# Kernel tuning notes

Hardware: AMD Instinct MI355X
Metric: run time of the kernel (lower is better)

Reference implementation:

```python
import jax, jax.numpy as jnp
import numpy as np

B, N, E, H = 8, 1500, 3000, 256
HOPS = 3


def setup_inputs() -> dict:
    key = jax.random.key(0)
    ks = jax.random.split(key, 9)
    node_state = jax.random.normal(ks[0], (B, N, H), jnp.float32)
    edge_vec = jax.random.normal(ks[1], (B, E, H), jnp.float32)
    # sparse-ish 0/1 incidence matrices (avg ~3 nonzeros per row)
    node2edge = (jax.random.uniform(ks[2], (B, E, N)) < 0.002).astype(jnp.float32)
    edge2node = (jax.random.uniform(ks[3], (B, N, E)) < 0.002).astype(jnp.float32)
    s = 1.0 / np.sqrt(H).astype(np.float32)
    W_max = jax.random.uniform(ks[4], (H, H), jnp.float32, -s, s)        # linear_max, no bias
    W_fz = jax.random.uniform(ks[5], (4 * H, H), jnp.float32, -s, s)     # gated fusion
    b_fz = jnp.zeros((H,), jnp.float32)
    W_z = jax.random.uniform(ks[6], (2 * H, H), jnp.float32, -s, s)      # GRU gates, no bias
    W_r = jax.random.uniform(ks[7], (2 * H, H), jnp.float32, -s, s)
    W_t = jax.random.uniform(ks[8], (2 * H, H), jnp.float32, -s, s)
    return dict(node_state=node_state, edge_vec=edge_vec, node2edge=node2edge,
                edge2node=edge2node, W_max=W_max, W_fz=W_fz, b_fz=b_fz,
                W_z=W_z, W_r=W_r, W_t=W_t)


def _msg_pass(node_state, edge_vec, n2e, e2n):
    # n2e: (B,E,N), e2n: (B,N,E)
    edge_emb = jnp.einsum('ben,bnh->beh', n2e, node_state) + edge_vec   # (B,E,H)
    norm = jnp.sum(e2n, axis=2, keepdims=True) + 1.0                     # self-loop degree norm
    return (jnp.einsum('bne,beh->bnh', e2n, edge_emb) + node_state) / norm


def _gated_fusion(h, x, W_fz, b_fz):
    z = jax.nn.sigmoid(jnp.concatenate([h, x, h * x, h - x], -1) @ W_fz + b_fz)
    return (1.0 - z) * h + z * x


def _gru_step(h, x, W_z, W_r, W_t):
    hx = jnp.concatenate([h, x], -1)
    z = jax.nn.sigmoid(hx @ W_z)
    r = jax.nn.sigmoid(hx @ W_r)
    t = jnp.tanh(jnp.concatenate([r * h, x], -1) @ W_t)
    return (1.0 - z) * h + z * t


def reference(node_state, edge_vec, node2edge, edge2node, W_max, W_fz, b_fz, W_z, W_r, W_t):
    n2e_T = jnp.swapaxes(node2edge, 1, 2)   # (B,N,E)
    e2n_T = jnp.swapaxes(edge2node, 1, 2)   # (B,E,N)
    for _ in range(HOPS):
        bw = _msg_pass(node_state, edge_vec, node2edge, edge2node)
        fw = _msg_pass(node_state, edge_vec, e2n_T, n2e_T)
        agg = _gated_fusion(fw, bw, W_fz, b_fz)
        node_state = _gru_step(node_state, agg, W_z, W_r, W_t)
    # graph max pool: linear then max over nodes
    graph_embedding = jnp.max(node_state @ W_max, axis=1)[None]  # (1,B,H)
    return jnp.swapaxes(node_state, 0, 1), graph_embedding       # (N,B,H), (1,B,H)
```

## Files before the change

### kernel.cpp

```cpp
#include <hip/hip_runtime.h>
#include <hip/hip_bf16.h>
#include <stdint.h>

#define Bb 8
#define Nn 1500
#define Ee 3000
#define Hh 256
#define NHOPS 3
#define CAP 32
#define Mrows (Bb*Nn)
#define BE (Bb*Ee)
#define BN (Bb*Nn)
#define TOTQ 9000000

typedef __bf16 bf16x8 __attribute__((ext_vector_type(8)));
typedef float f32x4 __attribute__((ext_vector_type(4)));

__device__ __forceinline__ float sigmoidf_(float x){ return 1.f/(1.f+__expf(-x)); }

__device__ __forceinline__ unsigned short f2b(float f){
  union { float f; unsigned int u; } x; x.f = f;
  unsigned int r = (x.u + 0x7fffu + ((x.u >> 16) & 1u)) >> 16;
  return (unsigned short)r;
}
__device__ __forceinline__ float b2f(unsigned short u){
  union { unsigned int u; float f; } x; x.u = ((unsigned int)u) << 16;
  return x.f;
}
__device__ __forceinline__ ushort4 pack4(float4 v){
  return make_ushort4(f2b(v.x), f2b(v.y), f2b(v.z), f2b(v.w));
}
__device__ __forceinline__ float4 unpack4(ushort4 u){
  return make_float4(b2f(u.x), b2f(u.y), b2f(u.z), b2f(u.w));
}
__device__ __forceinline__ unsigned fkey(float f){
  unsigned u = __float_as_uint(f);
  return (u & 0x80000000u) ? ~u : (u | 0x80000000u);
}

#define GLL16(g, l) __builtin_amdgcn_global_load_lds( \
    (const __attribute__((address_space(1))) unsigned int*)(g), \
    (__attribute__((address_space(3))) unsigned int*)(l), 16, 0, 0)

__device__ __forceinline__ void scan_proc(float4 vv, int t,
    int* __restrict__ Aidx, int* __restrict__ cntA, int* __restrict__ Didx, int* __restrict__ cntD,
    int* __restrict__ Bidx, int* __restrict__ cntB, int* __restrict__ Cidx, int* __restrict__ cntC) {
  if (vv.x == 0.f && vv.y == 0.f && vv.z == 0.f && vv.w == 0.f) return;
  int *rowIdx, *rowCnt, *colIdx, *colCnt;
  int g, q, R, C;
  if (t < TOTQ) {
    rowIdx = Aidx; rowCnt = cntA; colIdx = Didx; colCnt = cntD;
    R = Ee; C = Nn;
    g = t / 375; q = t - g * 375;
  } else {
    int tt = t - TOTQ;
    rowIdx = Bidx; rowCnt = cntB; colIdx = Cidx; colCnt = cntC;
    R = Nn; C = Ee;
    g = tt / 750; q = tt - g * 750;
  }
  int b = g / R;
  int r = g - b * R;
  int cbase = q * 4;
  #pragma unroll
  for (int j = 0; j < 4; ++j) {
    float vj = (j == 0) ? vv.x : (j == 1) ? vv.y : (j == 2) ? vv.z : vv.w;
    if (vj != 0.f) {
      int c = cbase + j;
      int rs = atomicAdd(&rowCnt[g], 1);
      if (rs < CAP) rowIdx[(size_t)g * CAP + rs] = c;
      int cs = atomicAdd(&colCnt[b * C + c], 1);
      if (cs < CAP) colIdx[(size_t)(b * C + c) * CAP + cs] = r;
    }
  }
}

__global__ void scan_kernel(const float4* __restrict__ n2e4, const float4* __restrict__ e2n4,
                            int* __restrict__ Aidx, int* __restrict__ cntA,
                            int* __restrict__ Didx, int* __restrict__ cntD,
                            int* __restrict__ Bidx, int* __restrict__ cntB,
                            int* __restrict__ Cidx, int* __restrict__ cntC) {
  int t0 = blockIdx.x * 1024 + threadIdx.x;
  float4 v[4];
  int ts[4];
  #pragma unroll
  for (int r2 = 0; r2 < 4; ++r2) {
    int t = t0 + r2 * 256;
    ts[r2] = t;
    const float4* p = (t < TOTQ) ? (n2e4 + t) : (e2n4 + (t - TOTQ));
    v[r2] = (t < 2 * TOTQ) ? *p : make_float4(0.f, 0.f, 0.f, 0.f);
  }
  __builtin_amdgcn_sched_barrier(0);
  #pragma unroll
  for (int r2 = 0; r2 < 4; ++r2)
    scan_proc(v[r2], ts[r2], Aidx, cntA, Didx, cntD, Bidx, cntB, Cidx, cntC);
}

__global__ void prep_kernel(const float* __restrict__ Wfz, const float* __restrict__ Wz,
                            const float* __restrict__ Wr, const float* __restrict__ Wt,
                            const float* __restrict__ Wmax,
                            unsigned short* __restrict__ WfzT, unsigned short* __restrict__ WzrT,
                            unsigned short* __restrict__ WtT, unsigned short* __restrict__ WmaxT,
                            const float* __restrict__ in_ns, unsigned short* __restrict__ nsb,
                            const float* __restrict__ in_ev, unsigned short* __restrict__ evb) {
  int bx = blockIdx.x;
  if (bx < 2560) {
    int t = bx * 256 + threadIdx.x;
    if (t < 196608) {
      int n = t / 768, k = t % 768;
      float v;
      if (k < 256)      v = Wfz[k * 256 + n] + Wfz[(k + 768) * 256 + n];
      else if (k < 512) v = Wfz[k * 256 + n] - Wfz[(k + 512) * 256 + n];
      else              v = Wfz[k * 256 + n];
      WfzT[t] = f2b(v);
    } else if (t < 458752) {
      int u = t - 196608;
      int j = u >> 9, k = u & 511;
      float v = (j < 256) ? Wz[k * 256 + j] : Wr[k * 256 + (j - 256)];
      WzrT[u] = f2b(v);
    } else if (t < 589824) {
      int u = t - 458752;
      int n = u >> 9, k = u & 511;
      WtT[u] = f2b(Wt[k * 256 + n]);
    } else if (t < 655360) {
      int u = t - 589824;
      int n = u >> 8, k = u & 255;
      WmaxT[u] = f2b(Wmax[k * 256 + n]);
    }
  } else if (bx < 3310) {
    int t0 = (bx - 2560) * 1024 + threadIdx.x;
    #pragma unroll
    for (int r = 0; r < 4; ++r) {
      int t = t0 + r * 256;
      ((ushort4*)nsb)[t] = pack4(((const float4*)in_ns)[t]);
    }
  } else {
    int t0 = (bx - 3310) * 1024 + threadIdx.x;
    #pragma unroll
    for (int r = 0; r < 4; ++r) {
      int t = t0 + r * 256;
      ((ushort4*)evb)[t] = pack4(((const float4*)in_ev)[t]);
    }
  }
}

__device__ __forceinline__ void sort_one(int* pp, int c) {
  if (c > CAP) c = CAP;
  int v[CAP];
  for (int j = 0; j < c; ++j) v[j] = pp[j];
  for (int j = 1; j < c; ++j) { int key = v[j]; int k = j - 1;
    while (k >= 0 && v[k] > key) { v[k+1] = v[k]; --k; } v[k+1] = key; }
  for (int j = 0; j < c; ++j) pp[j] = v[j];
}
__global__ void sort4_kernel(int* __restrict__ Cidx, const int* __restrict__ cntC,
                             int* __restrict__ Didx, const int* __restrict__ cntD,
                             int* __restrict__ Aidx, const int* __restrict__ cntA,
                             int* __restrict__ Bidx, const int* __restrict__ cntB) {
  int i = blockIdx.x * 256 + threadIdx.x;
  if (i < BE) sort_one(Cidx + (size_t)i * CAP, cntC[i]);
  else if (i < BE + BN) { int k = i - BE; sort_one(Didx + (size_t)k * CAP, cntD[k]); }
  else if (i < 2 * BE + BN) { int k = i - BE - BN; sort_one(Aidx + (size_t)k * CAP, cntA[k]); }
  else if (i < 2 * BE + 2 * BN) { int k = i - 2 * BE - BN; sort_one(Bidx + (size_t)k * CAP, cntB[k]); }
}

__global__ void edge_kernel(const ushort4* __restrict__ evb4, const ushort4* __restrict__ nsb4,
                            const int* __restrict__ Aidx, const int* __restrict__ Acnt,
                            const int* __restrict__ Cidx, const int* __restrict__ Ccnt,
                            ushort4* __restrict__ eb4, ushort4* __restrict__ ef4) {
  int w = __builtin_amdgcn_readfirstlane((int)(threadIdx.x >> 6));
  int be = blockIdx.x * 4 + w;
  int lane = threadIdx.x & 63;
  int b = be / Ee;
  int cA = min(Acnt[be], CAP), cC = min(Ccnt[be], CAP);
  const int* pA = Aidx + (size_t)be * CAP;
  const int* pC = Cidx + (size_t)be * CAP;
  float4 ev = unpack4(evb4[(size_t)be * 64 + lane]);
  float4 sA = ev, sC = ev;
  for (int i = 0; i < cA; ++i) {
    int n = pA[i];
    float4 t = unpack4(nsb4[((size_t)b * Nn + n) * 64 + lane]);
    sA.x += t.x; sA.y += t.y; sA.z += t.z; sA.w += t.w;
  }
  for (int i = 0; i < cC; ++i) {
    int n = pC[i];
    float4 t = unpack4(nsb4[((size_t)b * Nn + n) * 64 + lane]);
    sC.x += t.x; sC.y += t.y; sC.z += t.z; sC.w += t.w;
  }
  eb4[(size_t)be * 64 + lane] = pack4(sA);
  ef4[(size_t)be * 64 + lane] = pack4(sC);
}

__global__ void node_kernel(const float4* __restrict__ nsin4,
                            const ushort4* __restrict__ eb4, const ushort4* __restrict__ ef4,
                            const int* __restrict__ Bidx, const int* __restrict__ Bcnt,
                            const int* __restrict__ Didx, const int* __restrict__ Dcnt,
                            ushort4* __restrict__ Xfz4, ushort4* __restrict__ Xzr4) {
  int w = __builtin_amdgcn_readfirstlane((int)(threadIdx.x >> 6));
  int bn = blockIdx.x * 4 + w;
  int lane = threadIdx.x & 63;
  int b = bn / Nn;
  int rB = Bcnt[bn], rD = Dcnt[bn];
  int cB = min(rB, CAP), cD = min(rD, CAP);
  const int* pB = Bidx + (size_t)bn * CAP;
  const int* pD = Didx + (size_t)bn * CAP;
  float4 h0 = nsin4[(size_t)bn * 64 + lane];
  float4 sb = h0, sf = h0;
  for (int i = 0; i < cB; ++i) {
    int e = pB[i];
    float4 t = unpack4(eb4[((size_t)b * Ee + e) * 64 + lane]);
    sb.x += t.x; sb.y += t.y; sb.z += t.z; sb.w += t.w;
  }
  for (int i = 0; i < cD; ++i) {
    int e = pD[i];
    float4 t = unpack4(ef4[((size_t)b * Ee + e) * 64 + lane]);
    sf.x += t.x; sf.y += t.y; sf.z += t.z; sf.w += t.w;
  }
  float ib = 1.f / (1.f + (float)rB), idf = 1.f / (1.f + (float)rD);
  sb.x *= ib; sb.y *= ib; sb.z *= ib; sb.w *= ib;
  sf.x *= idf; sf.y *= idf; sf.z *= idf; sf.w *= idf;
  float4 prod = make_float4(sf.x*sb.x, sf.y*sb.y, sf.z*sb.z, sf.w*sb.w);
  size_t m = bn;
  Xfz4[m * 192 +   0 + lane] = pack4(sf);
  Xfz4[m * 192 +  64 + lane] = pack4(sb);
  Xfz4[m * 192 + 128 + lane] = pack4(prod);
  Xzr4[m * 128 + lane] = pack4(h0);
}

#define EPI_FZ   1
#define EPI_ZR   2
#define EPI_GRU  3
#define EPI_MAX  4

template<int EPI, int LAST>
__global__ __launch_bounds__(512) void gemm_kernel(
    const unsigned short* __restrict__ A, const unsigned short* __restrict__ WT,
    int M, int K,
    unsigned* __restrict__ gkey, const float* __restrict__ bfz,
    unsigned short* __restrict__ Xzr, unsigned short* __restrict__ zbuf,
    unsigned short* __restrict__ Xt,
    const float* __restrict__ nsin, float* __restrict__ nsout,
    unsigned short* __restrict__ nsbout)
{
  __shared__ unsigned short As[128 * 64];
  __shared__ unsigned short Bs[64 * 64];
  int m0 = blockIdx.x * 128, n0 = blockIdx.y * 64;
  int tid = threadIdx.x;
  int lane = tid & 63;
  int wid = __builtin_amdgcn_readfirstlane(tid >> 6);
  int wm = wid >> 1, wn = wid & 1;
  int p = lane >> 4;
  int q = lane & 7;
  int lr = lane >> 3;
  f32x4 acc[2][2] = {};
  for (int k0 = 0; k0 < K; k0 += 64) {
    {
      int rl0 = wid * 16 + lr;
      int gm0 = m0 + rl0; if (gm0 > M - 1) gm0 = M - 1;
      GLL16(A + (size_t)gm0 * K + k0 + ((q ^ (rl0 & 7)) << 3), &As[(wid * 16) * 64]);
      int rl1 = rl0 + 8;
      int gm1 = m0 + rl1; if (gm1 > M - 1) gm1 = M - 1;
      GLL16(A + (size_t)gm1 * K + k0 + ((q ^ (rl1 & 7)) << 3), &As[(wid * 16 + 8) * 64]);
      int rb = wid * 8 + lr;
      GLL16(WT + (size_t)(n0 + rb) * K + k0 + ((q ^ (rb & 7)) << 3), &Bs[(wid * 8) * 64]);
    }
    __syncthreads();
    #pragma unroll
    for (int kk = 0; kk < 64; kk += 32) {
      int cq = (kk >> 3) + p;
      int ra0 = wm * 32 + (lane & 15);
      int ra1 = ra0 + 16;
      int rb0 = wn * 32 + (lane & 15);
      int rb1 = rb0 + 16;
      bf16x8 a0 = *(const bf16x8*)&As[ra0 * 64 + ((cq ^ (ra0 & 7)) << 3)];
      bf16x8 a1 = *(const bf16x8*)&As[ra1 * 64 + ((cq ^ (ra1 & 7)) << 3)];
      bf16x8 b0 = *(const bf16x8*)&Bs[rb0 * 64 + ((cq ^ (rb0 & 7)) << 3)];
      bf16x8 b1 = *(const bf16x8*)&Bs[rb1 * 64 + ((cq ^ (rb1 & 7)) << 3)];
      acc[0][0] = __builtin_amdgcn_mfma_f32_16x16x32_bf16(a0, b0, acc[0][0], 0, 0, 0);
      acc[0][1] = __builtin_amdgcn_mfma_f32_16x16x32_bf16(a0, b1, acc[0][1], 0, 0, 0);
      acc[1][0] = __builtin_amdgcn_mfma_f32_16x16x32_bf16(a1, b0, acc[1][0], 0, 0, 0);
      acc[1][1] = __builtin_amdgcn_mfma_f32_16x16x32_bf16(a1, b1, acc[1][1], 0, 0, 0);
    }
    __syncthreads();
  }
  if (EPI == EPI_MAX) {
    #pragma unroll
    for (int mi = 0; mi < 2; ++mi)
    #pragma unroll
    for (int ni = 0; ni < 2; ++ni) {
      int mb = m0 + wm * 32 + mi * 16 + p * 4;
      int c = n0 + wn * 32 + ni * 16 + (lane & 15);
      if (mb >= M) continue;
      int b0 = mb / Nn, b3 = (mb + 3) / Nn;
      if (b0 == b3) {
        float mx = fmaxf(fmaxf(acc[mi][ni][0], acc[mi][ni][1]),
                         fmaxf(acc[mi][ni][2], acc[mi][ni][3]));
        atomicMax(&gkey[b0 * 256 + c], fkey(mx));
      } else {
        #pragma unroll
        for (int j = 0; j < 4; ++j)
          atomicMax(&gkey[((mb + j) / Nn) * 256 + c], fkey(acc[mi][ni][j]));
      }
    }
    return;
  }
  #pragma unroll
  for (int mi = 0; mi < 2; ++mi)
  #pragma unroll
  for (int ni = 0; ni < 2; ++ni)
  #pragma unroll
  for (int j = 0; j < 4; ++j) {
    int m = m0 + wm * 32 + mi * 16 + p * 4 + j;
    int c = n0 + wn * 32 + ni * 16 + (lane & 15);
    if (m >= M) continue;
    float v = acc[mi][ni][j];
    if (EPI == EPI_FZ) {
      float z = sigmoidf_(v + bfz[c]);
      float fw = b2f(A[(size_t)m * K + c]);
      float bw = b2f(A[(size_t)m * K + 256 + c]);
      unsigned short agg = f2b((1.f - z) * fw + z * bw);
      Xzr[(size_t)m * 512 + 256 + c] = agg;
      Xt[(size_t)m * 512 + 256 + c] = agg;
    } else if (EPI == EPI_ZR) {
      float s = sigmoidf_(v);
      if (c < 256) {
        zbuf[(size_t)m * 256 + c] = f2b(s);
      } else {
        int cz = c - 256;
        Xt[(size_t)m * 512 + cz] = f2b(s * nsin[(size_t)m * 256 + cz]);
      }
    } else {
      float t = tanhf(v);
      float zz = b2f(zbuf[(size_t)m * 256 + c]);
      float h = nsin[(size_t)m * 256 + c];
      float nh = (1.f - zz) * h + zz * t;
      nsbout[(size_t)m * 256 + c] = f2b(nh);
      if (LAST) {
        int bb = m / Nn, n = m - bb * Nn;
        nsout[((size_t)n * Bb + bb) * 256 + c] = nh;
      } else {
        nsout[(size_t)m * 256 + c] = nh;
      }
    }
  }
}

__global__ void maxfin_kernel(const unsigned* __restrict__ gkey, float* __restrict__ out) {
  int t = blockIdx.x * 256 + threadIdx.x;
  if (t >= Bb * Hh) return;
  unsigned k = gkey[t];
  unsigned u = (k & 0x80000000u) ? (k & 0x7fffffffu) : ~k;
  out[(size_t)Nn * Bb * Hh + t] = __uint_as_float(u);
}

extern "C" void kernel_launch(void* const* d_in, const int* in_sizes, int n_in,
                              void* d_out, int out_size, void* d_ws, size_t ws_size,
                              hipStream_t stream) {
  const float* in_ns   = (const float*)d_in[0];
  const float* in_ev   = (const float*)d_in[1];
  const float* in_n2e  = (const float*)d_in[2];
  const float* in_e2n  = (const float*)d_in[3];
  const float* in_wmax = (const float*)d_in[4];
  const float* in_wfz  = (const float*)d_in[5];
  const float* in_bfz  = (const float*)d_in[6];
  const float* in_wz   = (const float*)d_in[7];
  const float* in_wr   = (const float*)d_in[8];
  const float* in_wt   = (const float*)d_in[9];
  float* out = (float*)d_out;

  char* base = (char*)d_ws;
  size_t off = 0;
  auto alloc = [&](size_t bytes) -> void* {
    void* r = base + off;
    off = (off + bytes + 255) & ~(size_t)255;
    return r;
  };
  int* cnts = (int*)alloc((size_t)(2 * BE + 2 * BN) * 4);
  unsigned* gkey = (unsigned*)alloc(Bb * Hh * 4);
  int* cntC = cnts;
  int* cntD = cnts + BE;
  int* cntA = cnts + BE + BN;
  int* cntB = cnts + BE + BN + BE;
  int* Aidx = (int*)alloc((size_t)BE * CAP * 4);
  int* Bidx = (int*)alloc((size_t)BN * CAP * 4);
  int* Cidx = (int*)alloc((size_t)BE * CAP * 4);
  int* Didx = (int*)alloc((size_t)BN * CAP * 4);
  float* ns   = (float*)alloc((size_t)Mrows * Hh * 4);
  unsigned short* nsb = (unsigned short*)alloc((size_t)Mrows * Hh * 2);
  unsigned short* evb = (unsigned short*)alloc((size_t)BE * Hh * 2);
  unsigned short* eb = (unsigned short*)alloc((size_t)BE * Hh * 2);
  unsigned short* ef = (unsigned short*)alloc((size_t)BE * Hh * 2);
  unsigned short* Xfz = (unsigned short*)alloc((size_t)Mrows * 768 * 2);
  unsigned short* Xzr = (unsigned short*)alloc((size_t)Mrows * 512 * 2);
  unsigned short* Xt  = (unsigned short*)alloc((size_t)Mrows * 512 * 2);
  unsigned short* zbuf = (unsigned short*)alloc((size_t)Mrows * 256 * 2);
  unsigned short* WfzT  = (unsigned short*)alloc(256 * 768 * 2);
  unsigned short* WzrT  = (unsigned short*)alloc(512 * 512 * 2);
  unsigned short* WtT   = (unsigned short*)alloc(256 * 512 * 2);
  unsigned short* WmaxT = (unsigned short*)alloc(256 * 256 * 2);
  (void)ws_size; (void)in_sizes; (void)n_in; (void)out_size;

  hipMemsetAsync(cnts, 0, (size_t)(2 * BE + 2 * BN) * 4 + (size_t)Bb * Hh * 4, stream);

  scan_kernel<<<(2 * TOTQ + 1023) / 1024, 256, 0, stream>>>(
      (const float4*)in_n2e, (const float4*)in_e2n,
      Aidx, cntA, Didx, cntD, Bidx, cntB, Cidx, cntC);
  prep_kernel<<<4810, 256, 0, stream>>>(
      in_wfz, in_wz, in_wr, in_wt, in_wmax,
      WfzT, WzrT, WtT, WmaxT,
      in_ns, nsb, in_ev, evb);
  sort4_kernel<<<(2 * BE + 2 * BN + 255) / 256, 256, 0, stream>>>(
      Cidx, cntC, Didx, cntD, Aidx, cntA, Bidx, cntB);

  dim3 gFZ(94, 4), gZR(94, 8), gT(94, 4);
  for (int hop = 0; hop < NHOPS; ++hop) {
    const float* nsin = (hop == 0) ? in_ns : ns;
    edge_kernel<<<BE / 4, 256, 0, stream>>>((const ushort4*)evb, (const ushort4*)nsb,
        Aidx, cntA, Cidx, cntC, (ushort4*)eb, (ushort4*)ef);
    node_kernel<<<BN / 4, 256, 0, stream>>>((const float4*)nsin,
        (const ushort4*)eb, (const ushort4*)ef,
        Bidx, cntB, Didx, cntD, (ushort4*)Xfz, (ushort4*)Xzr);
    gemm_kernel<EPI_FZ, 0><<<gFZ, 512, 0, stream>>>(Xfz, WfzT, Mrows, 768,
        nullptr, in_bfz, Xzr, nullptr, Xt, nullptr, nullptr, nullptr);
    gemm_kernel<EPI_ZR, 0><<<gZR, 512, 0, stream>>>(Xzr, WzrT, Mrows, 512,
        nullptr, nullptr, nullptr, zbuf, Xt, nsin, nullptr, nullptr);
    if (hop < NHOPS - 1) {
      gemm_kernel<EPI_GRU, 0><<<gT, 512, 0, stream>>>(Xt, WtT, Mrows, 512,
          nullptr, nullptr, nullptr, zbuf, nullptr, nsin, ns, nsb);
    } else {
      gemm_kernel<EPI_GRU, 1><<<gT, 512, 0, stream>>>(Xt, WtT, Mrows, 512,
          nullptr, nullptr, nullptr, zbuf, nullptr, nsin, out, nsb);
    }
  }

  gemm_kernel<EPI_MAX, 0><<<gT, 512, 0, stream>>>(nsb, WmaxT, Mrows, 256,
      gkey, nullptr, nullptr, nullptr, nullptr, nullptr, nullptr, nullptr);
  maxfin_kernel<<<(Bb * Hh + 255) / 256, 256, 0, stream>>>(gkey, out);
}
```

Measured before the change: 443.1 us.

## Merge scan and prep kernels, split GEMM A operand, reduce max in LDS

Merges the incidence scan and weight/state conversion into one launch and loads the dense incidence matrices with nontemporal loads. The GEMMs now read their A operand from two separate buffers (nsb/aggb, rhb/aggb), so the node kernel and FZ epilogue no longer write duplicated concatenated copies into Xzr/Xt. The max-pool epilogue first reduces per block in LDS before issuing global atomics. Together these aim to cut memory traffic, one launch and atomic contention, at the cost of a more complex GEMM addressing path.

```diff
diff --git a/kernel.cpp b/kernel.cpp
--- a/kernel.cpp
+++ b/kernel.cpp
@@ -15,6 +15,7 @@
 
 typedef __bf16 bf16x8 __attribute__((ext_vector_type(8)));
 typedef float f32x4 __attribute__((ext_vector_type(4)));
+typedef float nf4 __attribute__((ext_vector_type(4)));
 
 __device__ __forceinline__ float sigmoidf_(float x){ return 1.f/(1.f+__expf(-x)); }
 
@@ -42,7 +43,7 @@
     (const __attribute__((address_space(1))) unsigned int*)(g), \
     (__attribute__((address_space(3))) unsigned int*)(l), 16, 0, 0)
 
-__device__ __forceinline__ void scan_proc(float4 vv, int t,
+__device__ __forceinline__ void scan_proc(nf4 vv, int t,
     int* __restrict__ Aidx, int* __restrict__ cntA, int* __restrict__ Didx, int* __restrict__ cntD,
     int* __restrict__ Bidx, int* __restrict__ cntB, int* __restrict__ Cidx, int* __restrict__ cntC) {
   if (vv.x == 0.f && vv.y == 0.f && vv.z == 0.f && vv.w == 0.f) return;
@@ -74,37 +75,37 @@
   }
 }
 
-__global__ void scan_kernel(const float4* __restrict__ n2e4, const float4* __restrict__ e2n4,
-                            int* __restrict__ Aidx, int* __restrict__ cntA,
-                            int* __restrict__ Didx, int* __restrict__ cntD,
-                            int* __restrict__ Bidx, int* __restrict__ cntB,
-                            int* __restrict__ Cidx, int* __restrict__ cntC) {
-  int t0 = blockIdx.x * 1024 + threadIdx.x;
-  float4 v[4];
-  int ts[4];
-  #pragma unroll
-  for (int r2 = 0; r2 < 4; ++r2) {
-    int t = t0 + r2 * 256;
-    ts[r2] = t;
-    const float4* p = (t < TOTQ) ? (n2e4 + t) : (e2n4 + (t - TOTQ));
-    v[r2] = (t < 2 * TOTQ) ? *p : make_float4(0.f, 0.f, 0.f, 0.f);
-  }
-  __builtin_amdgcn_sched_barrier(0);
-  #pragma unroll
-  for (int r2 = 0; r2 < 4; ++r2)
-    scan_proc(v[r2], ts[r2], Aidx, cntA, Didx, cntD, Bidx, cntB, Cidx, cntC);
-}
-
-__global__ void prep_kernel(const float* __restrict__ Wfz, const float* __restrict__ Wz,
-                            const float* __restrict__ Wr, const float* __restrict__ Wt,
-                            const float* __restrict__ Wmax,
-                            unsigned short* __restrict__ WfzT, unsigned short* __restrict__ WzrT,
-                            unsigned short* __restrict__ WtT, unsigned short* __restrict__ WmaxT,
-                            const float* __restrict__ in_ns, unsigned short* __restrict__ nsb,
-                            const float* __restrict__ in_ev, unsigned short* __restrict__ evb) {
+__global__ void preprocess_kernel(const nf4* __restrict__ n2e4, const nf4* __restrict__ e2n4,
+                                  int* __restrict__ Aidx, int* __restrict__ cntA,
+                                  int* __restrict__ Didx, int* __restrict__ cntD,
+                                  int* __restrict__ Bidx, int* __restrict__ cntB,
+                                  int* __restrict__ Cidx, int* __restrict__ cntC,
+                                  const float* __restrict__ Wfz, const float* __restrict__ Wz,
+                                  const float* __restrict__ Wr, const float* __restrict__ Wt,
+                                  const float* __restrict__ Wmax,
+                                  unsigned short* __restrict__ WfzT, unsigned short* __restrict__ WzrT,
+                                  unsigned short* __restrict__ WtT, unsigned short* __restrict__ WmaxT,
+                                  const float* __restrict__ in_ns, unsigned short* __restrict__ nsb,
+                                  const float* __restrict__ in_ev, unsigned short* __restrict__ evb) {
   int bx = blockIdx.x;
-  if (bx < 2560) {
-    int t = bx * 256 + threadIdx.x;
+  if (bx < 17580) {
+    int t0 = bx * 1024 + threadIdx.x;
+    nf4 v[4];
+    int ts[4];
+    #pragma unroll
+    for (int r2 = 0; r2 < 4; ++r2) {
+      int t = t0 + r2 * 256;
+      ts[r2] = t;
+      const nf4* p = (t < TOTQ) ? (n2e4 + t) : (e2n4 + (t - TOTQ));
+      if (t < 2 * TOTQ) v[r2] = __builtin_nontemporal_load(p);
+      else { v[r2].x = 0.f; v[r2].y = 0.f; v[r2].z = 0.f; v[r2].w = 0.f; }
+    }
+    __builtin_amdgcn_sched_barrier(0);
+    #pragma unroll
+    for (int r2 = 0; r2 < 4; ++r2)
+      scan_proc(v[r2], ts[r2], Aidx, cntA, Didx, cntD, Bidx, cntB, Cidx, cntC);
+  } else if (bx < 20140) {
+    int t = (bx - 17580) * 256 + threadIdx.x;
     if (t < 196608) {
       int n = t / 768, k = t % 768;
       float v;
@@ -126,15 +127,15 @@
       int n = u >> 8, k = u & 255;
       WmaxT[u] = f2b(Wmax[k * 256 + n]);
     }
-  } else if (bx < 3310) {
-    int t0 = (bx - 2560) * 1024 + threadIdx.x;
+  } else if (bx < 20890) {
+    int t0 = (bx - 20140) * 1024 + threadIdx.x;
     #pragma unroll
     for (int r = 0; r < 4; ++r) {
       int t = t0 + r * 256;
       ((ushort4*)nsb)[t] = pack4(((const float4*)in_ns)[t]);
     }
   } else {
-    int t0 = (bx - 3310) * 1024 + threadIdx.x;
+    int t0 = (bx - 20890) * 1024 + threadIdx.x;
     #pragma unroll
     for (int r = 0; r < 4; ++r) {
       int t = t0 + r * 256;
@@ -189,11 +190,11 @@
   ef4[(size_t)be * 64 + lane] = pack4(sC);
 }
 
-__global__ void node_kernel(const float4* __restrict__ nsin4,
+__global__ void node_kernel(const ushort4* __restrict__ nsb4,
                             const ushort4* __restrict__ eb4, const ushort4* __restrict__ ef4,
                             const int* __restrict__ Bidx, const int* __restrict__ Bcnt,
                             const int* __restrict__ Didx, const int* __restrict__ Dcnt,
-                            ushort4* __restrict__ Xfz4, ushort4* __restrict__ Xzr4) {
+                            ushort4* __restrict__ Xfz4) {
   int w = __builtin_amdgcn_readfirstlane((int)(threadIdx.x >> 6));
   int bn = blockIdx.x * 4 + w;
   int lane = threadIdx.x & 63;
@@ -202,7 +203,7 @@
   int cB = min(rB, CAP), cD = min(rD, CAP);
   const int* pB = Bidx + (size_t)bn * CAP;
   const int* pD = Didx + (size_t)bn * CAP;
-  float4 h0 = nsin4[(size_t)bn * 64 + lane];
+  float4 h0 = unpack4(nsb4[(size_t)bn * 64 + lane]);
   float4 sb = h0, sf = h0;
   for (int i = 0; i < cB; ++i) {
     int e = pB[i];
@@ -222,26 +223,27 @@
   Xfz4[m * 192 +   0 + lane] = pack4(sf);
   Xfz4[m * 192 +  64 + lane] = pack4(sb);
   Xfz4[m * 192 + 128 + lane] = pack4(prod);
-  Xzr4[m * 128 + lane] = pack4(h0);
-}
-
+}
+
+#define EPI_MAXR 0
 #define EPI_FZ   1
 #define EPI_ZR   2
 #define EPI_GRU  3
-#define EPI_MAX  4
-
-template<int EPI, int LAST>
+
+template<int EPI, int LAST, int SPLIT>
 __global__ __launch_bounds__(512) void gemm_kernel(
-    const unsigned short* __restrict__ A, const unsigned short* __restrict__ WT,
+    const unsigned short* __restrict__ A0, const unsigned short* __restrict__ A1,
+    const unsigned short* __restrict__ WT,
     int M, int K,
     unsigned* __restrict__ gkey, const float* __restrict__ bfz,
-    unsigned short* __restrict__ Xzr, unsigned short* __restrict__ zbuf,
-    unsigned short* __restrict__ Xt,
+    unsigned short* __restrict__ aggb, unsigned short* __restrict__ zbuf,
+    unsigned short* __restrict__ rhb,
     const float* __restrict__ nsin, float* __restrict__ nsout,
     unsigned short* __restrict__ nsbout)
 {
   __shared__ unsigned short As[128 * 64];
   __shared__ unsigned short Bs[64 * 64];
+  __shared__ unsigned redk[2][64];
   int m0 = blockIdx.x * 128, n0 = blockIdx.y * 64;
   int tid = threadIdx.x;
   int lane = tid & 63;
@@ -250,15 +252,19 @@
   int p = lane >> 4;
   int q = lane & 7;
   int lr = lane >> 3;
+  if (EPI == EPI_MAXR && tid < 128) redk[tid >> 6][tid & 63] = 0u;
   f32x4 acc[2][2] = {};
   for (int k0 = 0; k0 < K; k0 += 64) {
+    const unsigned short* srcA = A0;
+    int kA = k0, sA = K;
+    if (SPLIT) { sA = 256; if (k0 >= 256) { srcA = A1; kA = k0 - 256; } }
     {
       int rl0 = wid * 16 + lr;
       int gm0 = m0 + rl0; if (gm0 > M - 1) gm0 = M - 1;
-      GLL16(A + (size_t)gm0 * K + k0 + ((q ^ (rl0 & 7)) << 3), &As[(wid * 16) * 64]);
+      GLL16(srcA + (size_t)gm0 * sA + kA + ((q ^ (rl0 & 7)) << 3), &As[(wid * 16) * 64]);
       int rl1 = rl0 + 8;
       int gm1 = m0 + rl1; if (gm1 > M - 1) gm1 = M - 1;
-      GLL16(A + (size_t)gm1 * K + k0 + ((q ^ (rl1 & 7)) << 3), &As[(wid * 16 + 8) * 64]);
+      GLL16(srcA + (size_t)gm1 * sA + kA + ((q ^ (rl1 & 7)) << 3), &As[(wid * 16 + 8) * 64]);
       int rb = wid * 8 + lr;
       GLL16(WT + (size_t)(n0 + rb) * K + k0 + ((q ^ (rb & 7)) << 3), &Bs[(wid * 8) * 64]);
     }
@@ -281,23 +287,33 @@
     }
     __syncthreads();
   }
-  if (EPI == EPI_MAX) {
-    #pragma unroll
-    for (int mi = 0; mi < 2; ++mi)
+  if (EPI == EPI_MAXR) {
+    int blo = m0 / Nn;
+    int bnd = (blo + 1) * Nn;
     #pragma unroll
     for (int ni = 0; ni < 2; ++ni) {
-      int mb = m0 + wm * 32 + mi * 16 + p * 4;
-      int c = n0 + wn * 32 + ni * 16 + (lane & 15);
-      if (mb >= M) continue;
-      int b0 = mb / Nn, b3 = (mb + 3) / Nn;
-      if (b0 == b3) {
-        float mx = fmaxf(fmaxf(acc[mi][ni][0], acc[mi][ni][1]),
-                         fmaxf(acc[mi][ni][2], acc[mi][ni][3]));
-        atomicMax(&gkey[b0 * 256 + c], fkey(mx));
-      } else {
-        #pragma unroll
-        for (int j = 0; j < 4; ++j)
-          atomicMax(&gkey[((mb + j) / Nn) * 256 + c], fkey(acc[mi][ni][j]));
+      unsigned um0 = 0u, um1 = 0u;
+      #pragma unroll
+      for (int mi = 0; mi < 2; ++mi)
+      #pragma unroll
+      for (int j = 0; j < 4; ++j) {
+        int m = m0 + wm * 32 + mi * 16 + p * 4 + j;
+        if (m < M) {
+          unsigned k = fkey(acc[mi][ni][j]);
+          if (m >= bnd) um1 = max(um1, k); else um0 = max(um0, k);
+        }
+      }
+      int cl = wn * 32 + ni * 16 + (lane & 15);
+      if (um0) atomicMax(&redk[0][cl], um0);
+      if (um1) atomicMax(&redk[1][cl], um1);
+    }
+    __syncthreads();
+    if (tid < 128) {
+      int g = tid >> 6, cl = tid & 63;
+      unsigned k = redk[g][cl];
+      if (k) {
+        int mm = (g == 0) ? m0 : (m0 + 127 < M ? m0 + 127 : M - 1);
+        atomicMax(&gkey[(mm / Nn) * 256 + n0 + cl], k);
       }
     }
     return;
@@ -314,18 +330,16 @@
     float v = acc[mi][ni][j];
     if (EPI == EPI_FZ) {
       float z = sigmoidf_(v + bfz[c]);
-      float fw = b2f(A[(size_t)m * K + c]);
-      float bw = b2f(A[(size_t)m * K + 256 + c]);
-      unsigned short agg = f2b((1.f - z) * fw + z * bw);
-      Xzr[(size_t)m * 512 + 256 + c] = agg;
-      Xt[(size_t)m * 512 + 256 + c] = agg;
+      float fw = b2f(A0[(size_t)m * K + c]);
+      float bw = b2f(A0[(size_t)m * K + 256 + c]);
+      aggb[(size_t)m * 256 + c] = f2b((1.f - z) * fw + z * bw);
     } else if (EPI == EPI_ZR) {
       float s = sigmoidf_(v);
       if (c < 256) {
         zbuf[(size_t)m * 256 + c] = f2b(s);
       } else {
         int cz = c - 256;
-        Xt[(size_t)m * 512 + cz] = f2b(s * nsin[(size_t)m * 256 + cz]);
+        rhb[(size_t)m * 256 + cz] = f2b(s * nsin[(size_t)m * 256 + cz]);
       }
     } else {
       float t = tanhf(v);
@@ -389,8 +403,8 @@
   unsigned short* eb = (unsigned short*)alloc((size_t)BE * Hh * 2);
   unsigned short* ef = (unsigned short*)alloc((size_t)BE * Hh * 2);
   unsigned short* Xfz = (unsigned short*)alloc((size_t)Mrows * 768 * 2);
-  unsigned short* Xzr = (unsigned short*)alloc((size_t)Mrows * 512 * 2);
-  unsigned short* Xt  = (unsigned short*)alloc((size_t)Mrows * 512 * 2);
+  unsigned short* aggb = (unsigned short*)alloc((size_t)Mrows * 256 * 2);
+  unsigned short* rhb  = (unsigned short*)alloc((size_t)Mrows * 256 * 2);
   unsigned short* zbuf = (unsigned short*)alloc((size_t)Mrows * 256 * 2);
   unsigned short* WfzT  = (unsigned short*)alloc(256 * 768 * 2);
   unsigned short* WzrT  = (unsigned short*)alloc(512 * 512 * 2);
@@ -400,10 +414,9 @@
 
   hipMemsetAsync(cnts, 0, (size_t)(2 * BE + 2 * BN) * 4 + (size_t)Bb * Hh * 4, stream);
 
-  scan_kernel<<<(2 * TOTQ + 1023) / 1024, 256, 0, stream>>>(
-      (const float4*)in_n2e, (const float4*)in_e2n,
-      Aidx, cntA, Didx, cntD, Bidx, cntB, Cidx, cntC);
-  prep_kernel<<<4810, 256, 0, stream>>>(
+  preprocess_kernel<<<22390, 256, 0, stream>>>(
+      (const nf4*)in_n2e, (const nf4*)in_e2n,
+      Aidx, cntA, Didx, cntD, Bidx, cntB, Cidx, cntC,
       in_wfz, in_wz, in_wr, in_wt, in_wmax,
       WfzT, WzrT, WtT, WmaxT,
       in_ns, nsb, in_ev, evb);
@@ -415,23 +428,23 @@
     const float* nsin = (hop == 0) ? in_ns : ns;
     edge_kernel<<<BE / 4, 256, 0, stream>>>((const ushort4*)evb, (const ushort4*)nsb,
         Aidx, cntA, Cidx, cntC, (ushort4*)eb, (ushort4*)ef);
-    node_kernel<<<BN / 4, 256, 0, stream>>>((const float4*)nsin,
+    node_kernel<<<BN / 4, 256, 0, stream>>>((const ushort4*)nsb,
         (const ushort4*)eb, (const ushort4*)ef,
-        Bidx, cntB, Didx, cntD, (ushort4*)Xfz, (ushort4*)Xzr);
-    gemm_kernel<EPI_FZ, 0><<<gFZ, 512, 0, stream>>>(Xfz, WfzT, Mrows, 768,
-        nullptr, in_bfz, Xzr, nullptr, Xt, nullptr, nullptr, nullptr);
-    gemm_kernel<EPI_ZR, 0><<<gZR, 512, 0, stream>>>(Xzr, WzrT, Mrows, 512,
-        nullptr, nullptr, nullptr, zbuf, Xt, nsin, nullptr, nullptr);
+        Bidx, cntB, Didx, cntD, (ushort4*)Xfz);
+    gemm_kernel<EPI_FZ, 0, 0><<<gFZ, 512, 0, stream>>>(Xfz, nullptr, WfzT, Mrows, 768,
+        nullptr, in_bfz, aggb, nullptr, nullptr, nullptr, nullptr, nullptr);
+    gemm_kernel<EPI_ZR, 0, 1><<<gZR, 512, 0, stream>>>(nsb, aggb, WzrT, Mrows, 512,
+        nullptr, nullptr, nullptr, zbuf, rhb, nsin, nullptr, nullptr);
     if (hop < NHOPS - 1) {
-      gemm_kernel<EPI_GRU, 0><<<gT, 512, 0, stream>>>(Xt, WtT, Mrows, 512,
+      gemm_kernel<EPI_GRU, 0, 1><<<gT, 512, 0, stream>>>(rhb, aggb, WtT, Mrows, 512,
           nullptr, nullptr, nullptr, zbuf, nullptr, nsin, ns, nsb);
     } else {
-      gemm_kernel<EPI_GRU, 1><<<gT, 512, 0, stream>>>(Xt, WtT, Mrows, 512,
+      gemm_kernel<EPI_GRU, 1, 1><<<gT, 512, 0, stream>>>(rhb, aggb, WtT, Mrows, 512,
           nullptr, nullptr, nullptr, zbuf, nullptr, nsin, out, nsb);
     }
   }
 
-  gemm_kernel<EPI_MAX, 0><<<gT, 512, 0, stream>>>(nsb, WmaxT, Mrows, 256,
+  gemm_kernel<EPI_MAXR, 0, 0><<<gT, 512, 0, stream>>>(nsb, nullptr, WmaxT, Mrows, 256,
       gkey, nullptr, nullptr, nullptr, nullptr, nullptr, nullptr, nullptr);
   maxfin_kernel<<<(Bb * Hh + 255) / 256, 256, 0, stream>>>(gkey, out);
 }
```

New measurement: 387.2 us. 12.6% less time.
